# Performance work log

Measured on AMD Instinct MI355X. Metric: run time of the kernel, lower is better.

The kernel has to match this reference:

```python
import jax, jax.numpy as jnp
import numpy as np

V, E, H = 32000, 512, 1024   # vocab, embed, hidden
N, S = 64, 2048              # batch, encoder seq len


def setup_inputs() -> dict:
    key = jax.random.key(0)
    ks = jax.random.split(key, 12)
    s = 0.02
    inp = {
        # avoid padding_idx=0 so grads/embeds are nontrivial
        "prev_outputs": jax.random.randint(ks[0], (N, 1), 1, V),
        "prev_hn": jax.random.normal(ks[1], (1, N, H), jnp.float32),
        "prev_cn": jax.random.normal(ks[2], (1, N, H), jnp.float32),
        "encoder_hidden_states": jax.random.normal(ks[3], (N, S, H), jnp.float32),
        "emb_W": (jax.random.normal(ks[4], (V, E), jnp.float32) * s).at[0].set(0.0),  # padding_idx=0
        "w_ih": jax.random.normal(ks[5], (4 * H, E), jnp.float32) * s,
        "w_hh": jax.random.normal(ks[6], (4 * H, H), jnp.float32) * s,
        "b_ih": jax.random.normal(ks[7], (4 * H,), jnp.float32) * s,
        "b_hh": jax.random.normal(ks[8], (4 * H,), jnp.float32) * s,
        "fc_W": jax.random.normal(ks[9], (V, 2 * H), jnp.float32) * s,
        "fc_b": jax.random.normal(ks[10], (V,), jnp.float32) * s,
    }
    return inp


def reference(prev_outputs, prev_hn, prev_cn, encoder_hidden_states,
              emb_W, w_ih, w_hh, b_ih, b_hh, fc_W, fc_b):
    # embedding lookup: (N,1) -> (N,E) (seq_len==1 single decode step)
    x = emb_W[prev_outputs[:, 0]]                      # (N, E)
    h0 = prev_hn[0]                                    # (N, H)
    c0 = prev_cn[0]                                    # (N, H)
    # single LSTM step; PyTorch gate order i, f, g, o
    gates = x @ w_ih.T + b_ih + h0 @ w_hh.T + b_hh     # (N, 4H)
    i, f, g, o = jnp.split(gates, 4, axis=1)
    c = jax.nn.sigmoid(f) * c0 + jax.nn.sigmoid(i) * jnp.tanh(g)
    h = jax.nn.sigmoid(o) * jnp.tanh(c)                # (N, H) == squeezed LSTM out
    # raw dot alignment (no softmax, faithful to source)
    scores = jnp.einsum("nsh,nh->ns", encoder_hidden_states, h)   # (N, S)
    context = jnp.einsum("nsh,ns->nh", encoder_hidden_states, scores)  # (N, H)
    concat = jnp.concatenate([h, context], axis=1)     # (N, 2H)
    logits = concat @ fc_W.T + fc_b                    # (N, V)
    logp = jax.nn.log_softmax(logits, axis=1)
    return logp, h[None], c[None]
```

## Files before the change

kernel.cpp:

```cpp
#include <hip/hip_runtime.h>
#include <math.h>

#define V_ 32000
#define E_ 512
#define H_ 1024
#define N_ 64
#define S_ 2048

typedef short bf16x8 __attribute__((ext_vector_type(8)));
typedef float f32x4 __attribute__((ext_vector_type(4)));

__device__ __forceinline__ float sigmoidf_(float x) { return 1.0f / (1.0f + expf(-x)); }

__device__ __forceinline__ unsigned f2bf_u(float f) {
  unsigned a = __float_as_uint(f);
  return (a + 0x7fffu + ((a >> 16) & 1u)) >> 16;
}
__device__ __forceinline__ unsigned pk2(float lo, float hi) {
  return f2bf_u(lo) | (f2bf_u(hi) << 16);
}
__device__ __forceinline__ unsigned short f2bf(float f) { return (unsigned short)f2bf_u(f); }

__global__ __launch_bounds__(256) void k_gemm64t(
    const float* __restrict__ W1, const float* __restrict__ W2,
    const int* __restrict__ prev_out, const float* __restrict__ embW,
    const float* __restrict__ h0, float* __restrict__ Cpart, int klen) {
  const int t = threadIdx.x;
  const int j0 = blockIdx.x * 64;
  const int part = blockIdx.y;
  const int kbeg = part * klen;
  const int kend = kbeg + klen;

  __shared__ float zt[32][68];
  __shared__ float wt[32][68];

  const int tc = t & 15;
  const int tr = t >> 4;
  const int jw = t >> 2;
  const int kq = (t & 3) * 8;

  const int zrow = prev_out[jw];

  float acc[4][4];
#pragma unroll
  for (int i = 0; i < 4; i++)
#pragma unroll
    for (int j = 0; j < 4; j++) acc[i][j] = 0.f;

  for (int k0 = kbeg; k0 < kend; k0 += 32) {
    const float* zsrc;
    const float* wrow;
    if (k0 < E_) {
      zsrc = embW + (size_t)zrow * E_ + k0 + kq;
      wrow = W1 + (size_t)(j0 + jw) * E_ + k0 + kq;
    } else {
      zsrc = h0 + (size_t)jw * H_ + (k0 - E_) + kq;
      wrow = W2 + (size_t)(j0 + jw) * H_ + (k0 - E_) + kq;
    }
    float4 za = *(const float4*)(zsrc);
    float4 zb = *(const float4*)(zsrc + 4);
    float4 wa = *(const float4*)(wrow);
    float4 wb = *(const float4*)(wrow + 4);

    __syncthreads();
    zt[kq + 0][jw] = za.x; zt[kq + 1][jw] = za.y;
    zt[kq + 2][jw] = za.z; zt[kq + 3][jw] = za.w;
    zt[kq + 4][jw] = zb.x; zt[kq + 5][jw] = zb.y;
    zt[kq + 6][jw] = zb.z; zt[kq + 7][jw] = zb.w;
    wt[kq + 0][jw] = wa.x; wt[kq + 1][jw] = wa.y;
    wt[kq + 2][jw] = wa.z; wt[kq + 3][jw] = wa.w;
    wt[kq + 4][jw] = wb.x; wt[kq + 5][jw] = wb.y;
    wt[kq + 6][jw] = wb.z; wt[kq + 7][jw] = wb.w;
    __syncthreads();

#pragma unroll 8
    for (int k = 0; k < 32; k++) {
      float4 z = *(const float4*)(&zt[k][tc * 4]);
      float4 w = *(const float4*)(&wt[k][tr * 4]);
      acc[0][0] += w.x * z.x; acc[0][1] += w.x * z.y; acc[0][2] += w.x * z.z; acc[0][3] += w.x * z.w;
      acc[1][0] += w.y * z.x; acc[1][1] += w.y * z.y; acc[1][2] += w.y * z.z; acc[1][3] += w.y * z.w;
      acc[2][0] += w.z * z.x; acc[2][1] += w.z * z.y; acc[2][2] += w.z * z.z; acc[2][3] += w.z * z.w;
      acc[3][0] += w.w * z.x; acc[3][1] += w.w * z.y; acc[3][2] += w.w * z.z; acc[3][3] += w.w * z.w;
    }
  }

  float* cp = Cpart + (size_t)part * 4096 * 64;
#pragma unroll
  for (int nn = 0; nn < 4; nn++) {
    int n = tc * 4 + nn;
    float4 o = make_float4(acc[0][nn], acc[1][nn], acc[2][nn], acc[3][nn]);
    *(float4*)(cp + (size_t)n * 4096 + j0 + tr * 4) = o;
  }
}

__global__ __launch_bounds__(256) void k_lstm_fused(
    const float* __restrict__ gpart, const float* __restrict__ b_ih,
    const float* __restrict__ b_hh, const float* __restrict__ c0,
    float* __restrict__ out_h, float* __restrict__ out_c,
    unsigned short* __restrict__ concat_bf) {
  int idx = blockIdx.x * 256 + threadIdx.x;
  int n = idx >> 10, hh = idx & 1023;
  float g[4];
#pragma unroll
  for (int ga = 0; ga < 4; ga++) {
    float s = b_ih[ga * H_ + hh] + b_hh[ga * H_ + hh];
#pragma unroll
    for (int p = 0; p < 4; p++)
      s += gpart[((size_t)p * 64 + n) * 4096 + ga * H_ + hh];
    g[ga] = s;
  }
  float cv = sigmoidf_(g[1]) * c0[idx] + sigmoidf_(g[0]) * tanhf(g[2]);
  float hv = sigmoidf_(g[3]) * tanhf(cv);
  out_h[idx] = hv;
  out_c[idx] = cv;
  concat_bf[(size_t)n * 2048 + hh] = f2bf(hv);
}

__global__ __launch_bounds__(256) void k_attn(
    const float* __restrict__ enc, const float* __restrict__ h,
    float* __restrict__ ctxPart) {
  const int c = blockIdx.x;
  const int n = blockIdx.y;
  const int t = threadIdx.x, w = t >> 6, lane = t & 63;

  __shared__ float hs[H_];
  __shared__ float cbuf[4][H_];
  ((float4*)hs)[t] = ((const float4*)(h + (size_t)n * H_))[t];
  __syncthreads();

  const float4* hp = (const float4*)hs;
  float4 hv0 = hp[lane], hv1 = hp[64 + lane], hv2 = hp[128 + lane], hv3 = hp[192 + lane];

  float ca[16];
#pragma unroll
  for (int i = 0; i < 16; i++) ca[i] = 0.f;

  for (int si = w; si < 128; si += 4) {
    const int s = c * 128 + si;
    const float4* row = (const float4*)(enc + ((size_t)n * S_ + s) * H_);
    float4 e0 = row[lane], e1 = row[64 + lane], e2 = row[128 + lane], e3 = row[192 + lane];
    float d = e0.x * hv0.x + e0.y * hv0.y + e0.z * hv0.z + e0.w * hv0.w
            + e1.x * hv1.x + e1.y * hv1.y + e1.z * hv1.z + e1.w * hv1.w
            + e2.x * hv2.x + e2.y * hv2.y + e2.z * hv2.z + e2.w * hv2.w
            + e3.x * hv3.x + e3.y * hv3.y + e3.z * hv3.z + e3.w * hv3.w;
#pragma unroll
    for (int m = 32; m; m >>= 1) d += __shfl_xor(d, m, 64);
    ca[0]  += d * e0.x; ca[1]  += d * e0.y; ca[2]  += d * e0.z; ca[3]  += d * e0.w;
    ca[4]  += d * e1.x; ca[5]  += d * e1.y; ca[6]  += d * e1.z; ca[7]  += d * e1.w;
    ca[8]  += d * e2.x; ca[9]  += d * e2.y; ca[10] += d * e2.z; ca[11] += d * e2.w;
    ca[12] += d * e3.x; ca[13] += d * e3.y; ca[14] += d * e3.z; ca[15] += d * e3.w;
  }

  float4* cb = (float4*)&cbuf[w][0];
  cb[0 * 64 + lane] = make_float4(ca[0], ca[1], ca[2], ca[3]);
  cb[1 * 64 + lane] = make_float4(ca[4], ca[5], ca[6], ca[7]);
  cb[2 * 64 + lane] = make_float4(ca[8], ca[9], ca[10], ca[11]);
  cb[3 * 64 + lane] = make_float4(ca[12], ca[13], ca[14], ca[15]);
  __syncthreads();

  float4 a0 = ((const float4*)&cbuf[0][0])[t];
  float4 a1 = ((const float4*)&cbuf[1][0])[t];
  float4 a2 = ((const float4*)&cbuf[2][0])[t];
  float4 a3 = ((const float4*)&cbuf[3][0])[t];
  float4 r = make_float4(a0.x + a1.x + a2.x + a3.x, a0.y + a1.y + a2.y + a3.y,
                         a0.z + a1.z + a2.z + a3.z, a0.w + a1.w + a2.w + a3.w);
  ((float4*)ctxPart)[((size_t)(n * 16 + c)) * 256 + t] = r;
}

__global__ __launch_bounds__(256) void k_ctxreduce_bf(
    const float* __restrict__ ctxPart, unsigned short* __restrict__ concat_bf) {
  int idx = blockIdx.x * 256 + threadIdx.x;
  int n = idx >> 10, hh = idx & 1023;
  float s = 0.f;
  for (int c = 0; c < 16; c++) s += ctxPart[((size_t)(n * 16 + c)) * H_ + hh];
  concat_bf[(size_t)n * 2048 + H_ + hh] = f2bf(s);
}

__global__ __launch_bounds__(256) void k_fc_mfma(
    const float* __restrict__ W, const unsigned short* __restrict__ Zbf,
    const float* __restrict__ bias, float* __restrict__ outNV,
    float* __restrict__ statsPart) {
  const int t = threadIdx.x;
  const int v0 = blockIdx.x * 64;
  const int w = t >> 6, lane = t & 63;
  __shared__ __align__(16) unsigned char smem[16384];

  f32x4 acc[4] = {{0.f,0.f,0.f,0.f},{0.f,0.f,0.f,0.f},{0.f,0.f,0.f,0.f},{0.f,0.f,0.f,0.f}};

  const int ar = t >> 2;
  const int ak = (t & 3) * 16;
  const float* aptr = W + (size_t)(v0 + ar) * 2048 + ak;
  const unsigned aslot0 = (unsigned)(ak >> 3);
  const unsigned awoff0 = ar * 128 + (((aslot0)     * 16) ^ ((ar & 7) << 4));
  const unsigned awoff1 = ar * 128 + (((aslot0 + 1) * 16) ^ ((ar & 7) << 4));
  const int bn0 = t >> 3;
  const int bs = t & 7;
  const unsigned bwoff0 = 8192 + bn0 * 128        + ((bs * 16) ^ ((bn0 & 7) << 4));
  const unsigned bwoff1 = 8192 + (bn0 + 32) * 128 + ((bs * 16) ^ (((bn0 + 32) & 7) << 4));

  const int arow = (w << 4) + (lane & 15);
  const int ksub = lane >> 4;
  const unsigned aro[2] = {
    (unsigned)(arow * 128 + (((0 * 4 + ksub) * 16) ^ ((arow & 7) << 4))),
    (unsigned)(arow * 128 + (((1 * 4 + ksub) * 16) ^ ((arow & 7) << 4)))};
  unsigned bro[2][4];
#pragma unroll
  for (int kh = 0; kh < 2; kh++)
#pragma unroll
    for (int nf = 0; nf < 4; nf++) {
      int brow = nf * 16 + (lane & 15);
      bro[kh][nf] = 8192 + brow * 128 + (((kh * 4 + ksub) * 16) ^ ((brow & 7) << 4));
    }

  float4 a0 = ((const float4*)aptr)[0];
  float4 a1 = ((const float4*)aptr)[1];
  float4 a2 = ((const float4*)aptr)[2];
  float4 a3 = ((const float4*)aptr)[3];
  uint4 bv0 = *(const uint4*)(Zbf + (size_t)bn0 * 2048 + bs * 8);
  uint4 bv1 = *(const uint4*)(Zbf + (size_t)(bn0 + 32) * 2048 + bs * 8);

  for (int k0 = 0; k0 < 2048; k0 += 64) {
    __syncthreads();
    uint4 pa0, pa1;
    pa0.x = pk2(a0.x, a0.y); pa0.y = pk2(a0.z, a0.w);
    pa0.z = pk2(a1.x, a1.y); pa0.w = pk2(a1.z, a1.w);
    pa1.x = pk2(a2.x, a2.y); pa1.y = pk2(a2.z, a2.w);
    pa1.z = pk2(a3.x, a3.y); pa1.w = pk2(a3.z, a3.w);
    *(uint4*)(smem + awoff0) = pa0;
    *(uint4*)(smem + awoff1) = pa1;
    *(uint4*)(smem + bwoff0) = bv0;
    *(uint4*)(smem + bwoff1) = bv1;
    if (k0 + 64 < 2048) {
      const float* ap = aptr + k0 + 64;
      a0 = ((const float4*)ap)[0];
      a1 = ((const float4*)ap)[1];
      a2 = ((const float4*)ap)[2];
      a3 = ((const float4*)ap)[3];
      bv0 = *(const uint4*)(Zbf + (size_t)bn0 * 2048 + (k0 + 64) + bs * 8);
      bv1 = *(const uint4*)(Zbf + (size_t)(bn0 + 32) * 2048 + (k0 + 64) + bs * 8);
    }
    __syncthreads();
#pragma unroll
    for (int kh = 0; kh < 2; kh++) {
      bf16x8 af = *(const bf16x8*)(smem + aro[kh]);
#pragma unroll
      for (int nf = 0; nf < 4; nf++) {
        bf16x8 bfr = *(const bf16x8*)(smem + bro[kh][nf]);
        acc[nf] = __builtin_amdgcn_mfma_f32_16x16x32_bf16(af, bfr, acc[nf], 0, 0, 0);
      }
    }
  }

  const int vrow = v0 + (w << 4) + ((lane >> 4) << 2);
  float4 b4 = *(const float4*)(bias + vrow);
  float vals[4][4];
#pragma unroll
  for (int nf = 0; nf < 4; nf++) {
    int n = nf * 16 + (lane & 15);
    vals[nf][0] = acc[nf][0] + b4.x; vals[nf][1] = acc[nf][1] + b4.y;
    vals[nf][2] = acc[nf][2] + b4.z; vals[nf][3] = acc[nf][3] + b4.w;
    *(float4*)(outNV + (size_t)n * V_ + vrow) =
        make_float4(vals[nf][0], vals[nf][1], vals[nf][2], vals[nf][3]);
  }

  __syncthreads();
  float* mx   = (float*)smem;
  float* sm   = (float*)(smem + 4096);
  float* bmax = (float*)(smem + 8192);
  const int cidx = w * 4 + (lane >> 4);
#pragma unroll
  for (int nf = 0; nf < 4; nf++) {
    int n = nf * 16 + (lane & 15);
    float m = fmaxf(fmaxf(vals[nf][0], vals[nf][1]), fmaxf(vals[nf][2], vals[nf][3]));
    mx[n * 16 + cidx] = m;
  }
  __syncthreads();
  if (t < 64) {
    float m = mx[t * 16];
#pragma unroll
    for (int i = 1; i < 16; i++) m = fmaxf(m, mx[t * 16 + i]);
    bmax[t] = m;
  }
  __syncthreads();
#pragma unroll
  for (int nf = 0; nf < 4; nf++) {
    int n = nf * 16 + (lane & 15);
    float M = bmax[n];
    float s = expf(vals[nf][0] - M) + expf(vals[nf][1] - M) +
              expf(vals[nf][2] - M) + expf(vals[nf][3] - M);
    sm[n * 16 + cidx] = s;
  }
  __syncthreads();
  if (t < 64) {
    float s = 0.f;
#pragma unroll
    for (int i = 0; i < 16; i++) s += sm[t * 16 + i];
    statsPart[(size_t)t * 1024 + blockIdx.x * 2]     = bmax[t];
    statsPart[(size_t)t * 1024 + blockIdx.x * 2 + 1] = s;
  }
}

__global__ __launch_bounds__(256) void k_logp_merged(
    float* __restrict__ logits, const float* __restrict__ statsPart) {
  const int n = blockIdx.y, t = threadIdx.x;
  const float2* sp = (const float2*)(statsPart + (size_t)n * 1024);

  float m = -INFINITY, s = 0.f;
#pragma unroll
  for (int rep = 0; rep < 2; rep++) {
    int p = rep * 256 + t;
    if (p < 500) {
      float2 e = sp[p];
      if (e.x > m) { s = s * expf(m - e.x) + e.y; m = e.x; }
      else         { s += e.y * expf(e.x - m); }
    }
  }
  __shared__ float ms[256], ss[256];
  ms[t] = m; ss[t] = s;
  __syncthreads();
  for (int off = 128; off; off >>= 1) {
    if (t < off) {
      float m2 = ms[t + off], s2 = ss[t + off];
      float M = fmaxf(ms[t], m2);
      ss[t] = ss[t] * expf(ms[t] - M) + s2 * expf(m2 - M);
      ms[t] = M;
    }
    __syncthreads();
  }
  const float sub = ms[0] + logf(ss[0]);

  const int v4 = blockIdx.x * 256 + t;
  if (v4 < V_ / 4) {
    float4* p = (float4*)(logits + (size_t)n * V_) + v4;
    float4 x = *p;
    *p = make_float4(x.x - sub, x.y - sub, x.z - sub, x.w - sub);
  }
}

extern "C" void kernel_launch(void* const* d_in, const int* in_sizes, int n_in,
                              void* d_out, int out_size, void* d_ws, size_t ws_size,
                              hipStream_t stream) {
  const int*   prev_out = (const int*)d_in[0];
  const float* h0   = (const float*)d_in[1];
  const float* c0   = (const float*)d_in[2];
  const float* enc  = (const float*)d_in[3];
  const float* embW = (const float*)d_in[4];
  const float* w_ih = (const float*)d_in[5];
  const float* w_hh = (const float*)d_in[6];
  const float* b_ih = (const float*)d_in[7];
  const float* b_hh = (const float*)d_in[8];
  const float* fc_W = (const float*)d_in[9];
  const float* fc_b = (const float*)d_in[10];

  float* out = (float*)d_out;
  float* logp  = out;
  float* out_h = out + (size_t)N_ * V_;
  float* out_c = out_h + (size_t)N_ * H_;

  char* wsb = (char*)d_ws;
  float* gpart   = (float*)wsb; wsb += (size_t)4 * 4096 * 64 * 4;
  float* ctxPart = (float*)wsb; wsb += (size_t)16 * 64 * H_ * 4;
  unsigned short* concat_bf = (unsigned short*)wsb; wsb += (size_t)64 * 2048 * 2;
  float* statsPart = (float*)wsb; wsb += (size_t)64 * 1024 * 4;

  k_gemm64t<<<dim3(4096 / 64, 4), 256, 0, stream>>>(
      w_ih, w_hh, prev_out, embW, h0, gpart, 384);
  k_lstm_fused<<<64 * H_ / 256, 256, 0, stream>>>(gpart, b_ih, b_hh, c0,
                                                  out_h, out_c, concat_bf);
  k_attn<<<dim3(16, 64), 256, 0, stream>>>(enc, out_h, ctxPart);
  k_ctxreduce_bf<<<64 * H_ / 256, 256, 0, stream>>>(ctxPart, concat_bf);
  k_fc_mfma<<<V_ / 64, 256, 0, stream>>>(fc_W, concat_bf, fc_b, logp, statsPart);
  k_logp_merged<<<dim3((V_ / 4 + 255) / 256, N_), 256, 0, stream>>>(logp, statsPart);
}
```

Measured before the change: 189.0 us.

## Load FC GEMM MFMA fragments directly from global memory, drop LDS staging

```diff
diff --git a/kernel.cpp b/kernel.cpp
--- a/kernel.cpp
+++ b/kernel.cpp
@@ -183,94 +183,53 @@
   const int t = threadIdx.x;
   const int v0 = blockIdx.x * 64;
   const int w = t >> 6, lane = t & 63;
-  __shared__ __align__(16) unsigned char smem[16384];
+  const int row = lane & 15;
+  const int ksub = lane >> 4;
 
   f32x4 acc[4] = {{0.f,0.f,0.f,0.f},{0.f,0.f,0.f,0.f},{0.f,0.f,0.f,0.f},{0.f,0.f,0.f,0.f}};
 
-  const int ar = t >> 2;
-  const int ak = (t & 3) * 16;
-  const float* aptr = W + (size_t)(v0 + ar) * 2048 + ak;
-  const unsigned aslot0 = (unsigned)(ak >> 3);
-  const unsigned awoff0 = ar * 128 + (((aslot0)     * 16) ^ ((ar & 7) << 4));
-  const unsigned awoff1 = ar * 128 + (((aslot0 + 1) * 16) ^ ((ar & 7) << 4));
-  const int bn0 = t >> 3;
-  const int bs = t & 7;
-  const unsigned bwoff0 = 8192 + bn0 * 128        + ((bs * 16) ^ ((bn0 & 7) << 4));
-  const unsigned bwoff1 = 8192 + (bn0 + 32) * 128 + ((bs * 16) ^ (((bn0 + 32) & 7) << 4));
-
-  const int arow = (w << 4) + (lane & 15);
-  const int ksub = lane >> 4;
-  const unsigned aro[2] = {
-    (unsigned)(arow * 128 + (((0 * 4 + ksub) * 16) ^ ((arow & 7) << 4))),
-    (unsigned)(arow * 128 + (((1 * 4 + ksub) * 16) ^ ((arow & 7) << 4)))};
-  unsigned bro[2][4];
-#pragma unroll
-  for (int kh = 0; kh < 2; kh++)
-#pragma unroll
-    for (int nf = 0; nf < 4; nf++) {
-      int brow = nf * 16 + (lane & 15);
-      bro[kh][nf] = 8192 + brow * 128 + (((kh * 4 + ksub) * 16) ^ ((brow & 7) << 4));
-    }
-
-  float4 a0 = ((const float4*)aptr)[0];
-  float4 a1 = ((const float4*)aptr)[1];
-  float4 a2 = ((const float4*)aptr)[2];
-  float4 a3 = ((const float4*)aptr)[3];
-  uint4 bv0 = *(const uint4*)(Zbf + (size_t)bn0 * 2048 + bs * 8);
-  uint4 bv1 = *(const uint4*)(Zbf + (size_t)(bn0 + 32) * 2048 + bs * 8);
-
-  for (int k0 = 0; k0 < 2048; k0 += 64) {
-    __syncthreads();
-    uint4 pa0, pa1;
-    pa0.x = pk2(a0.x, a0.y); pa0.y = pk2(a0.z, a0.w);
-    pa0.z = pk2(a1.x, a1.y); pa0.w = pk2(a1.z, a1.w);
-    pa1.x = pk2(a2.x, a2.y); pa1.y = pk2(a2.z, a2.w);
-    pa1.z = pk2(a3.x, a3.y); pa1.w = pk2(a3.z, a3.w);
-    *(uint4*)(smem + awoff0) = pa0;
-    *(uint4*)(smem + awoff1) = pa1;
-    *(uint4*)(smem + bwoff0) = bv0;
-    *(uint4*)(smem + bwoff1) = bv1;
-    if (k0 + 64 < 2048) {
-      const float* ap = aptr + k0 + 64;
-      a0 = ((const float4*)ap)[0];
-      a1 = ((const float4*)ap)[1];
-      a2 = ((const float4*)ap)[2];
-      a3 = ((const float4*)ap)[3];
-      bv0 = *(const uint4*)(Zbf + (size_t)bn0 * 2048 + (k0 + 64) + bs * 8);
-      bv1 = *(const uint4*)(Zbf + (size_t)(bn0 + 32) * 2048 + (k0 + 64) + bs * 8);
-    }
-    __syncthreads();
-#pragma unroll
-    for (int kh = 0; kh < 2; kh++) {
-      bf16x8 af = *(const bf16x8*)(smem + aro[kh]);
-#pragma unroll
-      for (int nf = 0; nf < 4; nf++) {
-        bf16x8 bfr = *(const bf16x8*)(smem + bro[kh][nf]);
-        acc[nf] = __builtin_amdgcn_mfma_f32_16x16x32_bf16(af, bfr, acc[nf], 0, 0, 0);
-      }
-    }
-  }
-
-  const int vrow = v0 + (w << 4) + ((lane >> 4) << 2);
+  const float* ap = W + (size_t)(v0 + (w << 4) + row) * 2048 + ksub * 8;
+  const unsigned short* bp = Zbf + (size_t)row * 2048 + ksub * 8;
+
+#pragma unroll 4
+  for (int ks = 0; ks < 64; ks++) {
+    const float* a = ap + ks * 32;
+    float4 a0 = ((const float4*)a)[0];
+    float4 a1 = ((const float4*)a)[1];
+    const unsigned short* b = bp + ks * 32;
+    uint4 b0 = *(const uint4*)(b);
+    uint4 b1 = *(const uint4*)(b + 16 * 2048);
+    uint4 b2 = *(const uint4*)(b + 32 * 2048);
+    uint4 b3 = *(const uint4*)(b + 48 * 2048);
+    uint4 pa;
+    pa.x = pk2(a0.x, a0.y); pa.y = pk2(a0.z, a0.w);
+    pa.z = pk2(a1.x, a1.y); pa.w = pk2(a1.z, a1.w);
+    bf16x8 af = *(bf16x8*)&pa;
+    acc[0] = __builtin_amdgcn_mfma_f32_16x16x32_bf16(af, *(bf16x8*)&b0, acc[0], 0, 0, 0);
+    acc[1] = __builtin_amdgcn_mfma_f32_16x16x32_bf16(af, *(bf16x8*)&b1, acc[1], 0, 0, 0);
+    acc[2] = __builtin_amdgcn_mfma_f32_16x16x32_bf16(af, *(bf16x8*)&b2, acc[2], 0, 0, 0);
+    acc[3] = __builtin_amdgcn_mfma_f32_16x16x32_bf16(af, *(bf16x8*)&b3, acc[3], 0, 0, 0);
+  }
+
+  const int vrow = v0 + (w << 4) + (ksub << 2);
   float4 b4 = *(const float4*)(bias + vrow);
   float vals[4][4];
 #pragma unroll
   for (int nf = 0; nf < 4; nf++) {
-    int n = nf * 16 + (lane & 15);
+    int n = nf * 16 + row;
     vals[nf][0] = acc[nf][0] + b4.x; vals[nf][1] = acc[nf][1] + b4.y;
     vals[nf][2] = acc[nf][2] + b4.z; vals[nf][3] = acc[nf][3] + b4.w;
     *(float4*)(outNV + (size_t)n * V_ + vrow) =
         make_float4(vals[nf][0], vals[nf][1], vals[nf][2], vals[nf][3]);
   }
 
-  __syncthreads();
-  float* mx   = (float*)smem;
-  float* sm   = (float*)(smem + 4096);
-  float* bmax = (float*)(smem + 8192);
-  const int cidx = w * 4 + (lane >> 4);
+  __shared__ float mx[64 * 16];
+  __shared__ float sm[64 * 16];
+  __shared__ float bmax[64];
+  const int cidx = w * 4 + ksub;
 #pragma unroll
   for (int nf = 0; nf < 4; nf++) {
-    int n = nf * 16 + (lane & 15);
+    int n = nf * 16 + row;
     float m = fmaxf(fmaxf(vals[nf][0], vals[nf][1]), fmaxf(vals[nf][2], vals[nf][3]));
     mx[n * 16 + cidx] = m;
   }
@@ -284,7 +243,7 @@
   __syncthreads();
 #pragma unroll
   for (int nf = 0; nf < 4; nf++) {
-    int n = nf * 16 + (lane & 15);
+    int n = nf * 16 + row;
     float M = bmax[n];
     float s = expf(vals[nf][0] - M) + expf(vals[nf][1] - M) +
               expf(vals[nf][2] - M) + expf(vals[nf][3] - M);
```

New measurement: 233.3 us. +23.4%, slower.
